# Kernel tuning notes

Measured on AMD Instinct MI355X. Metric: run time of the kernel, lower is better.

Reference implementation:

```python
import jax, jax.numpy as jnp
import numpy as np

HEAD_DIM = 64
N_HEADS = 12
N_KV_HEADS = 4
N_REP = N_HEADS // N_KV_HEADS  # 3


def _rope(x, cos, sin):
    # x: [B, S, H, D]; cos/sin: [1, S, D//2] -> broadcast over heads
    x2 = x.reshape(*x.shape[:-1], -1, 2)          # [B,S,H,D/2,2]
    x_r, x_i = x2[..., 0], x2[..., 1]
    c = cos[:, :, None, :]                         # [1,S,1,D/2]
    s = sin[:, :, None, :]
    o_r = x_r * c - x_i * s
    o_i = x_r * s + x_i * c
    return jnp.stack([o_r, o_i], axis=-1).reshape(x.shape)


def setup_inputs() -> dict:
    key = jax.random.key(0)
    ks = jax.random.split(key, 6)
    B, S, H = 4, 2048, 768
    hidden_state = jax.random.normal(ks[0], (B, S, H), dtype=jnp.float32)
    # true RoPE frequencies (theta=10000) for positions 0..S-1
    inv_freq = 1.0 / (10000.0 ** (np.arange(0, HEAD_DIM, 2, dtype=np.float32) / HEAD_DIM))
    ang = np.arange(S, dtype=np.float32)[:, None] * inv_freq[None, :]  # [S, D/2]
    freqs_cos = jnp.asarray(np.cos(ang))[None]     # [1,S,32]
    freqs_sin = jnp.asarray(np.sin(ang))[None]
    sc = 0.02
    wq = jax.random.normal(ks[1], (768, 768), dtype=jnp.float32) * sc
    wk = jax.random.normal(ks[2], (256, 768), dtype=jnp.float32) * sc
    wv = jax.random.normal(ks[3], (256, 768), dtype=jnp.float32) * sc
    wo = jax.random.normal(ks[4], (768, 768), dtype=jnp.float32) * sc
    return {"hidden_state": hidden_state, "freqs_cos": freqs_cos, "freqs_sin": freqs_sin,
            "wq": wq, "wk": wk, "wv": wv, "wo": wo}


def reference(hidden_state, freqs_cos, freqs_sin, wq, wk, wv, wo):
    B, S, _ = hidden_state.shape
    q = (hidden_state @ wq.T).reshape(B, S, N_HEADS, HEAD_DIM)
    k = (hidden_state @ wk.T).reshape(B, S, N_KV_HEADS, HEAD_DIM)
    v = (hidden_state @ wv.T).reshape(B, S, N_KV_HEADS, HEAD_DIM)
    q = _rope(q, freqs_cos, freqs_sin)
    k = _rope(k, freqs_cos, freqs_sin)
    # repeat_kv: [B,S,KV,D] -> [B,S,KV*n_rep,D]
    k = jnp.repeat(k, N_REP, axis=2)
    v = jnp.repeat(v, N_REP, axis=2)
    q = q.transpose(0, 2, 1, 3)  # [B,H,S,D]
    k = k.transpose(0, 2, 1, 3)
    v = v.transpose(0, 2, 1, 3)
    scores = jnp.einsum('bhqd,bhkd->bhqk', q, k) / np.sqrt(HEAD_DIM).astype(np.float32)
    mask = jnp.triu(jnp.full((S, S), -jnp.inf, dtype=scores.dtype), k=1)
    scores = scores + mask
    attn = jax.nn.softmax(scores.astype(jnp.float32), axis=-1).astype(q.dtype)
    # dropout is inference-off (identity)
    out = jnp.einsum('bhqk,bhkd->bhqd', attn, v)
    out = out.transpose(0, 2, 1, 3).reshape(B, S, N_HEADS * HEAD_DIM)
    return out @ wo.T, attn
```

## Files before the change

### kernel.cpp

```cpp
#include <hip/hip_runtime.h>
#include <hip/hip_bf16.h>
#include <stdint.h>


typedef __bf16 bf16x8 __attribute__((ext_vector_type(8)));
typedef float  f32x4  __attribute__((ext_vector_type(4)));

#define B_    4
#define S_    2048
#define H_    768
#define NH_Q  12
#define NKV_  4
#define D_    64
#define MROWS (B_ * S_)
#define NQKV  1280

__device__ __forceinline__ f32x4 mfma16(bf16x8 a, bf16x8 b, f32x4 c) {
  return __builtin_amdgcn_mfma_f32_16x16x32_bf16(a, b, c, 0, 0, 0);
}

__device__ __forceinline__ void st_nt4(float* p, f32x4 v) {
  __builtin_nontemporal_store(v, (f32x4*)p);
}

__device__ __forceinline__ uint32_t pk2(float a, float b) {
  __bf16 x = (__bf16)a, y = (__bf16)b;
  uint16_t xu = __builtin_bit_cast(uint16_t, x);
  uint16_t yu = __builtin_bit_cast(uint16_t, y);
  return (uint32_t)xu | ((uint32_t)yu << 16);
}
__device__ __forceinline__ float bl(uint32_t u) {
  uint32_t t = u << 16; return __builtin_bit_cast(float, t);
}
__device__ __forceinline__ float bh(uint32_t u) {
  uint32_t t = u & 0xffff0000u; return __builtin_bit_cast(float, t);
}

__global__ void cast_all(const float* __restrict__ X, const float* __restrict__ wq,
                         const float* __restrict__ wo, const float* __restrict__ wk,
                         const float* __restrict__ wv,
                         __bf16* __restrict__ Xb, __bf16* __restrict__ wqb,
                         __bf16* __restrict__ wob, __bf16* __restrict__ wkb,
                         __bf16* __restrict__ wvb) {
  int i = blockIdx.x * 256 + threadIdx.x;
  const int nX = MROWS * 768 / 8;
  const int nW = 768 * 768 / 8;
  const int nK = 256 * 768 / 8;
  const float* s; __bf16* d; int off;
  if (i < nX)                    { s = X;  d = Xb;  off = i; }
  else if (i < nX + nW)          { s = wq; d = wqb; off = i - nX; }
  else if (i < nX + 2 * nW)      { s = wo; d = wob; off = i - nX - nW; }
  else if (i < nX + 2 * nW + nK) { s = wk; d = wkb; off = i - nX - 2 * nW; }
  else if (i < nX + 2 * nW + 2 * nK) { s = wv; d = wvb; off = i - nX - 2 * nW - nK; }
  else return;
  const float4* sp = (const float4*)s + (size_t)off * 2;
  float4 a = sp[0], b = sp[1];
  bf16x8 o;
  o[0] = (__bf16)a.x; o[1] = (__bf16)a.y; o[2] = (__bf16)a.z; o[3] = (__bf16)a.w;
  o[4] = (__bf16)b.x; o[5] = (__bf16)b.y; o[6] = (__bf16)b.z; o[7] = (__bf16)b.w;
  *((bf16x8*)d + off) = o;
}

__global__ __launch_bounds__(256) void gemm_qkv(const __bf16* __restrict__ A,
                                                const __bf16* __restrict__ Wq,
                                                const __bf16* __restrict__ Wk,
                                                const __bf16* __restrict__ Wv,
                                                float* __restrict__ C) {
  const int K = 768;
  __shared__ __bf16 As[128 * 32];
  __shared__ __bf16 Bs[128 * 32];
  const int m0 = blockIdx.x * 128, n0 = blockIdx.y * 128;
  const __bf16* W;
  int nl;
  if (n0 < 768)       { W = Wq; nl = n0; }
  else if (n0 < 1024) { W = Wk; nl = n0 - 768; }
  else                { W = Wv; nl = n0 - 1024; }
  const int tid = threadIdx.x, lane = tid & 63, w = tid >> 6;
  const int wm = w >> 1, wn = w & 1;
  const int ql = lane & 15, grp = lane >> 4;
  const int srow = tid >> 1, shalf = tid & 1;
  const int sw = (srow >> 1) & 3;
  const int kc0 = (shalf * 2) ^ sw, kc1 = (shalf * 2 + 1) ^ sw;

  f32x4 acc[4][4] = {};

  for (int k0 = 0; k0 < K; k0 += 32) {
    bf16x8 av0 = *(const bf16x8*)(A + (size_t)(m0 + srow) * K + k0 + shalf * 16);
    bf16x8 av1 = *(const bf16x8*)(A + (size_t)(m0 + srow) * K + k0 + shalf * 16 + 8);
    bf16x8 bv0 = *(const bf16x8*)(W + (size_t)(nl + srow) * K + k0 + shalf * 16);
    bf16x8 bv1 = *(const bf16x8*)(W + (size_t)(nl + srow) * K + k0 + shalf * 16 + 8);
    __syncthreads();
    *(bf16x8*)(As + srow * 32 + kc0 * 8) = av0;
    *(bf16x8*)(As + srow * 32 + kc1 * 8) = av1;
    *(bf16x8*)(Bs + srow * 32 + kc0 * 8) = bv0;
    *(bf16x8*)(Bs + srow * 32 + kc1 * 8) = bv1;
    __syncthreads();

    bf16x8 af[4], bf_[4];
#pragma unroll
    for (int i = 0; i < 4; i++) {
      int row = wm * 64 + i * 16 + ql;
      int kc = grp ^ ((row >> 1) & 3);
      af[i] = *(const bf16x8*)(As + row * 32 + kc * 8);
    }
#pragma unroll
    for (int j = 0; j < 4; j++) {
      int row = wn * 64 + j * 16 + ql;
      int kc = grp ^ ((row >> 1) & 3);
      bf_[j] = *(const bf16x8*)(Bs + row * 32 + kc * 8);
    }
#pragma unroll
    for (int i = 0; i < 4; i++)
#pragma unroll
      for (int j = 0; j < 4; j++)
        acc[i][j] = mfma16(af[i], bf_[j], acc[i][j]);
  }

#pragma unroll
  for (int i = 0; i < 4; i++)
#pragma unroll
    for (int j = 0; j < 4; j++)
#pragma unroll
      for (int r = 0; r < 4; r++) {
        int row = m0 + wm * 64 + i * 16 + grp * 4 + r;
        int col = n0 + wn * 64 + j * 16 + ql;
        C[(size_t)row * NQKV + col] = acc[i][j][r];
      }
}

__global__ __launch_bounds__(256) void gemm_xwT(const __bf16* __restrict__ A,
                                                const __bf16* __restrict__ W,
                                                float* __restrict__ C,
                                                int M, int N, int K) {
  __shared__ __bf16 As[128 * 32];
  __shared__ __bf16 Bs[128 * 32];
  const int m0 = blockIdx.x * 128, n0 = blockIdx.y * 128;
  const int tid = threadIdx.x, lane = tid & 63, w = tid >> 6;
  const int wm = w >> 1, wn = w & 1;
  const int ql = lane & 15, grp = lane >> 4;
  const int srow = tid >> 1, shalf = tid & 1;
  const int sw = (srow >> 1) & 3;
  const int kc0 = (shalf * 2) ^ sw, kc1 = (shalf * 2 + 1) ^ sw;

  f32x4 acc[4][4] = {};

  for (int k0 = 0; k0 < K; k0 += 32) {
    bf16x8 av0 = *(const bf16x8*)(A + (size_t)(m0 + srow) * K + k0 + shalf * 16);
    bf16x8 av1 = *(const bf16x8*)(A + (size_t)(m0 + srow) * K + k0 + shalf * 16 + 8);
    bf16x8 bv0 = *(const bf16x8*)(W + (size_t)(n0 + srow) * K + k0 + shalf * 16);
    bf16x8 bv1 = *(const bf16x8*)(W + (size_t)(n0 + srow) * K + k0 + shalf * 16 + 8);
    __syncthreads();
    *(bf16x8*)(As + srow * 32 + kc0 * 8) = av0;
    *(bf16x8*)(As + srow * 32 + kc1 * 8) = av1;
    *(bf16x8*)(Bs + srow * 32 + kc0 * 8) = bv0;
    *(bf16x8*)(Bs + srow * 32 + kc1 * 8) = bv1;
    __syncthreads();

    bf16x8 af[4], bf_[4];
#pragma unroll
    for (int i = 0; i < 4; i++) {
      int row = wm * 64 + i * 16 + ql;
      int kc = grp ^ ((row >> 1) & 3);
      af[i] = *(const bf16x8*)(As + row * 32 + kc * 8);
    }
#pragma unroll
    for (int j = 0; j < 4; j++) {
      int row = wn * 64 + j * 16 + ql;
      int kc = grp ^ ((row >> 1) & 3);
      bf_[j] = *(const bf16x8*)(Bs + row * 32 + kc * 8);
    }
#pragma unroll
    for (int i = 0; i < 4; i++)
#pragma unroll
      for (int j = 0; j < 4; j++)
        acc[i][j] = mfma16(af[i], bf_[j], acc[i][j]);
  }

#pragma unroll
  for (int i = 0; i < 4; i++)
#pragma unroll
    for (int j = 0; j < 4; j++)
#pragma unroll
      for (int r = 0; r < 4; r++) {
        int row = m0 + wm * 64 + i * 16 + grp * 4 + r;
        int col = n0 + wn * 64 + j * 16 + ql;
        C[(size_t)row * N + col] = acc[i][j][r];
      }
}

__global__ void rope_both(const float* __restrict__ QKV, const float* __restrict__ fc,
                          const float* __restrict__ fs, __bf16* __restrict__ Qb,
                          __bf16* __restrict__ Kb) {
  int idx = blockIdx.x * 256 + threadIdx.x;
  const int NQp = MROWS * NH_Q * 32;
  int NH, colOff;
  __bf16* dst;
  float scale;
  if (idx < NQp) {
    NH = NH_Q; colOff = 0; dst = Qb; scale = 0.125f * 1.44269504f;
  } else {
    idx -= NQp;
    NH = NKV_; colOff = 768; dst = Kb; scale = 1.0f;
  }
  int t = idx & 31;
  int h = (idx >> 5) % NH;
  int row = idx / (32 * NH);
  int s = row & (S_ - 1), b = row >> 11;
  float x0 = QKV[(size_t)row * NQKV + colOff + h * 64 + 2 * t];
  float x1 = QKV[(size_t)row * NQKV + colOff + h * 64 + 2 * t + 1];
  float c = fc[s * 32 + t], sn = fs[s * 32 + t];
  float o0 = (x0 * c - x1 * sn) * scale;
  float o1 = (x0 * sn + x1 * c) * scale;
  __bf16* d = dst + (((size_t)(b * NH + h) * S_ + s) * 64 + 2 * t);
  d[0] = (__bf16)o0;
  d[1] = (__bf16)o1;
}

__global__ void transpose_v(const float* __restrict__ QKV, __bf16* __restrict__ VT) {
  __shared__ float tile[64][65];
  int rt = blockIdx.x;
  int ct = blockIdx.y;
  int r0 = rt * 64, c0 = ct * 64;
  int tx = threadIdx.x & 63, ty = threadIdx.x >> 6;
#pragma unroll
  for (int rep = 0; rep < 16; rep++) {
    int rr = rep * 4 + ty;
    tile[rr][tx] = QKV[(size_t)(r0 + rr) * NQKV + 1024 + c0 + tx];
  }
  __syncthreads();
  int b = r0 >> 11;
  int s0 = r0 & (S_ - 1);
#pragma unroll
  for (int rep = 0; rep < 16; rep++) {
    int dr = rep * 4 + ty;
    int d = c0 + dr;
    int kv = d >> 6, dd = d & 63;
    VT[(((size_t)(b * NKV_ + kv) * 64 + dd) * S_) + s0 + tx] = (__bf16)tile[tx][dr];
  }
}

template <int MAXC>
__device__ __forceinline__ void attn_part(
    int g, int b, int h, int w, int lane,
    const __bf16* __restrict__ Q, const __bf16* __restrict__ Kp,
    const __bf16* __restrict__ Vp, float* __restrict__ attn,
    __bf16* __restrict__ O, float (*lsum_s)[16], f32x4 (*obuf)[4]) {
  const int ql = lane & 15, grp = lane >> 4;
  const int qr0 = g * 16;
  const int nch = (g >> 1) + 1;
  const int i_q = qr0 + ql;
  const __bf16* Qp = Q + ((size_t)(b * NH_Q + h) * S_ + qr0) * 64;
  float* attnp = attn + ((size_t)(b * NH_Q + h) * S_ + qr0) * S_;

  bf16x8 bq0 = *(const bf16x8*)(Qp + ql * 64 + grp * 8);
  bf16x8 bq1 = *(const bf16x8*)(Qp + ql * 64 + 32 + grp * 8);

  uint32_t p[MAXC][4];
  float lsum = 0.f;
  f32x4 opv[4] = {};

#pragma unroll
  for (int c = 0; c < MAXC; c++) {
    const int j = w + 4 * c;
    if (j < nch) {
      const int j0 = j * 32;
      bf16x8 k0 = *(const bf16x8*)(Kp + (size_t)(j0 + ql) * 64 + grp * 8);
      bf16x8 k1 = *(const bf16x8*)(Kp + (size_t)(j0 + ql) * 64 + 32 + grp * 8);
      bf16x8 k2 = *(const bf16x8*)(Kp + (size_t)(j0 + 16 + ql) * 64 + grp * 8);
      bf16x8 k3 = *(const bf16x8*)(Kp + (size_t)(j0 + 16 + ql) * 64 + 32 + grp * 8);
      bf16x8 v0 = *(const bf16x8*)(Vp + (size_t)(0 * 16 + ql) * S_ + j0 + grp * 8);
      bf16x8 v1 = *(const bf16x8*)(Vp + (size_t)(1 * 16 + ql) * S_ + j0 + grp * 8);
      bf16x8 v2 = *(const bf16x8*)(Vp + (size_t)(2 * 16 + ql) * S_ + j0 + grp * 8);
      bf16x8 v3 = *(const bf16x8*)(Vp + (size_t)(3 * 16 + ql) * S_ + j0 + grp * 8);
      f32x4 s0 = {}, s1 = {};
      s0 = mfma16(k0, bq0, s0);
      s0 = mfma16(k1, bq1, s0);
      s1 = mfma16(k2, bq0, s1);
      s1 = mfma16(k3, bq1, s1);
      float e[8];
      if (j == nch - 1) {
#pragma unroll
        for (int r = 0; r < 4; r++) {
          int ja = j0 + grp * 4 + r, jb = j0 + 16 + grp * 4 + r;
          e[r]     = (ja <= i_q) ? exp2f(s0[r]) : 0.f;
          e[4 + r] = (jb <= i_q) ? exp2f(s1[r]) : 0.f;
        }
      } else {
#pragma unroll
        for (int r = 0; r < 4; r++) {
          e[r]     = exp2f(s0[r]);
          e[4 + r] = exp2f(s1[r]);
        }
      }
#pragma unroll
      for (int r = 0; r < 8; r++) lsum += e[r];
      p[c][0] = pk2(e[0], e[1]);
      p[c][1] = pk2(e[2], e[3]);
      p[c][2] = pk2(e[4], e[5]);
      p[c][3] = pk2(e[6], e[7]);

      int srcA = ql + 32 * (grp & 1);
      int srcB = srcA + 16;
      uint32_t A0 = __shfl(p[c][0], srcA), A1 = __shfl(p[c][1], srcA);
      uint32_t A2 = __shfl(p[c][2], srcA), A3 = __shfl(p[c][3], srcA);
      uint32_t B0 = __shfl(p[c][0], srcB), B1 = __shfl(p[c][1], srcB);
      uint32_t B2 = __shfl(p[c][2], srcB), B3 = __shfl(p[c][3], srcB);
      bool hi = (grp >> 1) != 0;
      union { bf16x8 v; uint32_t u[4]; } pu;
      pu.u[0] = hi ? A2 : A0;
      pu.u[1] = hi ? A3 : A1;
      pu.u[2] = hi ? B2 : B0;
      pu.u[3] = hi ? B3 : B1;
      opv[0] = mfma16(pu.v, v0, opv[0]);
      opv[1] = mfma16(pu.v, v1, opv[1]);
      opv[2] = mfma16(pu.v, v2, opv[2]);
      opv[3] = mfma16(pu.v, v3, opv[3]);
    }
  }

  lsum += __shfl_xor(lsum, 16);
  lsum += __shfl_xor(lsum, 32);
  if (lane < 16) lsum_s[w][ql] = lsum;
  f32x4* ob = obuf[w * 64 + lane];
  ob[0] = opv[0]; ob[1] = opv[1]; ob[2] = opv[2]; ob[3] = opv[3];
  __syncthreads();
  const float rinv = 1.f / (lsum_s[0][ql] + lsum_s[1][ql] + lsum_s[2][ql] + lsum_s[3][ql]);

  {
    const int dt = w;
    f32x4 acc = obuf[0 * 64 + lane][dt];
    acc += obuf[1 * 64 + lane][dt];
    acc += obuf[2 * 64 + lane][dt];
    acc += obuf[3 * 64 + lane][dt];
    __bf16* Op = O + ((size_t)(b * S_) + qr0) * H_ + h * 64;
#pragma unroll
    for (int r = 0; r < 4; r++) {
      int row = grp * 4 + r;
      float rr = 1.f / (lsum_s[0][row] + lsum_s[1][row] + lsum_s[2][row] + lsum_s[3][row]);
      Op[(size_t)row * H_ + dt * 16 + ql] = (__bf16)(acc[r] * rr);
    }
  }

#pragma unroll
  for (int c = 0; c < MAXC; c++) {
    const int j = w + 4 * c;
    if (j < nch) {
      const int j0 = j * 32;
      f32x4 q0, q1;
      q0[0] = bl(p[c][0]); q0[1] = bh(p[c][0]); q0[2] = bl(p[c][1]); q0[3] = bh(p[c][1]);
      q1[0] = bl(p[c][2]); q1[1] = bh(p[c][2]); q1[2] = bl(p[c][3]); q1[3] = bh(p[c][3]);
#pragma unroll
      for (int r = 0; r < 4; r++) { q0[r] *= rinv; q1[r] *= rinv; }
      st_nt4(attnp + (size_t)ql * S_ + j0 + grp * 4, q0);
      st_nt4(attnp + (size_t)ql * S_ + j0 + 16 + grp * 4, q1);
    }
  }

  const int jz = nch * 32;
  const int tid = w * 64 + lane;
  const f32x4 z4 = {0.f, 0.f, 0.f, 0.f};
#pragma unroll 1
  for (int rr = 0; rr < 16; rr++) {
    float* rowp = attnp + (size_t)rr * S_;
    for (int jj = jz + tid * 4; jj < S_; jj += 1024) st_nt4(rowp + jj, z4);
  }
  __syncthreads();
}

__global__ __launch_bounds__(256) void attn_kernel(const __bf16* __restrict__ Q,
                                                   const __bf16* __restrict__ Kb,
                                                   const __bf16* __restrict__ VT,
                                                   float* __restrict__ attn,
                                                   __bf16* __restrict__ O) {
  __shared__ float lsum_s[4][16];
  __shared__ f32x4 obuf[4 * 64][4];
  const int bid = blockIdx.x;
  const int r = bid & 7;
  const int qd = bid >> 3;
  const int x = qd & 63;
  const int idx6 = qd >> 6;
  const int g48 = idx6 * 8 + r;
  const int h = g48 >> 2, b = g48 & 3;
  const int lane = threadIdx.x & 63, w = threadIdx.x >> 6;
  const int kv = h / 3;
  const __bf16* Kp = Kb + (size_t)(b * NKV_ + kv) * S_ * 64;
  const __bf16* Vp = VT + (size_t)(b * NKV_ + kv) * 64 * S_;

  attn_part<8>(x, b, h, w, lane, Q, Kp, Vp, attn, O, lsum_s, obuf);
  attn_part<16>(127 - x, b, h, w, lane, Q, Kp, Vp, attn, O, lsum_s, obuf);
}

extern "C" void kernel_launch(void* const* d_in, const int* in_sizes, int n_in,
                              void* d_out, int out_size, void* d_ws, size_t ws_size,
                              hipStream_t stream) {
  (void)in_sizes; (void)n_in;
  const float* X  = (const float*)d_in[0];
  const float* fc = (const float*)d_in[1];
  const float* fs = (const float*)d_in[2];
  const float* wq = (const float*)d_in[3];
  const float* wk = (const float*)d_in[4];
  const float* wv = (const float*)d_in[5];
  const float* wo = (const float*)d_in[6];
  float* out0 = (float*)d_out;
  float* attn = out0 + (size_t)B_ * S_ * H_;

  char* p = (char*)d_ws;
  auto take = [&](size_t bytes) -> char* {
    char* r = p;
    p += (bytes + 255) & ~(size_t)255;
    return r;
  };
  __bf16* wqbf = (__bf16*)take((size_t)768 * 768 * 2);
  __bf16* wkbf = (__bf16*)take((size_t)256 * 768 * 2);
  __bf16* wvbf = (__bf16*)take((size_t)256 * 768 * 2);
  __bf16* wobf = (__bf16*)take((size_t)768 * 768 * 2);
  __bf16* Qbf  = (__bf16*)take((size_t)MROWS * 768 * 2);
  __bf16* Kbf  = (__bf16*)take((size_t)MROWS * 256 * 2);
  __bf16* VTbf = (__bf16*)take((size_t)MROWS * 256 * 2);
  __bf16* Obf  = (__bf16*)take((size_t)MROWS * 768 * 2);
  size_t used = (size_t)(p - (char*)d_ws);

  const size_t XBF_B  = (size_t)MROWS * 768 * 2;
  const size_t QKV_B  = (size_t)MROWS * NQKV * 4;
  const size_t TEMP_B = XBF_B + QKV_B;

  char* tp;
  if (used + TEMP_B + 1024 <= ws_size) {
    tp = p;
  } else {
    tp = (char*)(((uintptr_t)((char*)d_out + (size_t)out_size * 4 - TEMP_B)) & ~(uintptr_t)255);
  }
  __bf16* Xbf  = (__bf16*)tp;  tp += XBF_B;
  float*  QKVf = (float*)tp;

  {
    const int total8 = MROWS * 768 / 8 + 2 * (768 * 768 / 8) + 2 * (256 * 768 / 8);
    cast_all<<<(total8 + 255) / 256, 256, 0, stream>>>(X, wq, wo, wk, wv,
                                                       Xbf, wqbf, wobf, wkbf, wvbf);
  }

  gemm_qkv<<<dim3(MROWS / 128, NQKV / 128), 256, 0, stream>>>(Xbf, wqbf, wkbf, wvbf, QKVf);

  {
    const int totalPairs = MROWS * NH_Q * 32 + MROWS * NKV_ * 32;
    rope_both<<<(totalPairs + 255) / 256, 256, 0, stream>>>(QKVf, fc, fs, Qbf, Kbf);
  }
  transpose_v<<<dim3(MROWS / 64, 4), 256, 0, stream>>>(QKVf, VTbf);

  attn_kernel<<<dim3(48 * 64), 256, 0, stream>>>(Qbf, Kbf, VTbf, attn, Obf);

  gemm_xwT<<<dim3(MROWS / 128, 768 / 128), 256, 0, stream>>>(Obf, wobf, out0, MROWS, 768, 768);
}
```

Baseline: 323.0 us.

## Double-buffer GEMM tiles via direct global-to-LDS loads; split attention into two passes

The QKV and output projection GEMMs now use two LDS buffers filled by global_load_lds, so the next K tile loads while MFMAs run on the current one, and each K step needs one barrier instead of two. The attention row kernel now computes all exponentials and the row sum first, then in a second pass loads V, does the PV MFMAs and writes the normalized attention probabilities. The goal is to hide global latency in the GEMMs and interleave the large attention-matrix stores with compute. The cost is double the LDS per GEMM block, and a dependence on the direct-to-LDS lane layout matching the swizzle.

```diff
diff --git a/kernel.cpp b/kernel.cpp
--- a/kernel.cpp
+++ b/kernel.cpp
@@ -14,6 +14,7 @@
 #define D_    64
 #define MROWS (B_ * S_)
 #define NQKV  1280
+#define TILE_E (128 * 32)
 
 __device__ __forceinline__ f32x4 mfma16(bf16x8 a, bf16x8 b, f32x4 c) {
   return __builtin_amdgcn_mfma_f32_16x16x32_bf16(a, b, c, 0, 0, 0);
@@ -34,6 +35,12 @@
 }
 __device__ __forceinline__ float bh(uint32_t u) {
   uint32_t t = u & 0xffff0000u; return __builtin_bit_cast(float, t);
+}
+
+__device__ __forceinline__ void gload_lds16(const __bf16* g, __bf16* l) {
+  __builtin_amdgcn_global_load_lds(
+      (const __attribute__((address_space(1))) void*)g,
+      (__attribute__((address_space(3))) void*)l, 16, 0, 0);
 }
 
 __global__ void cast_all(const float* __restrict__ X, const float* __restrict__ wq,
@@ -61,131 +68,122 @@
   *((bf16x8*)d + off) = o;
 }
 
+struct GemmPtrs {
+  const __bf16 *gA0, *gA1, *gB0, *gB1;
+};
+
+__device__ __forceinline__ GemmPtrs make_ptrs(const __bf16* A, const __bf16* W,
+                                              int m0, int n0, int K, int tid) {
+  GemmPtrs gp;
+  int c0 = tid, c1 = 256 + tid;
+  int sr0 = c0 >> 2, kc0 = (c0 & 3) ^ ((sr0 >> 1) & 3);
+  int sr1 = c1 >> 2, kc1 = (c1 & 3) ^ ((sr1 >> 1) & 3);
+  gp.gA0 = A + (size_t)(m0 + sr0) * K + kc0 * 8;
+  gp.gA1 = A + (size_t)(m0 + sr1) * K + kc1 * 8;
+  gp.gB0 = W + (size_t)(n0 + sr0) * K + kc0 * 8;
+  gp.gB1 = W + (size_t)(n0 + sr1) * K + kc1 * 8;
+  return gp;
+}
+
+__device__ __forceinline__ void gemm_stage(GemmPtrs gp, int k0,
+                                           __bf16* As, __bf16* Bs, int tid) {
+  __bf16* lA0 = As + (size_t)(tid & ~63) * 8;
+  __bf16* lB0 = Bs + (size_t)(tid & ~63) * 8;
+  gload_lds16(gp.gA0 + k0, lA0);
+  gload_lds16(gp.gA1 + k0, lA0 + 256 * 8);
+  gload_lds16(gp.gB0 + k0, lB0);
+  gload_lds16(gp.gB1 + k0, lB0 + 256 * 8);
+}
+
+__device__ __forceinline__ void gemm_core(GemmPtrs gp, int K,
+                                          __bf16* As, __bf16* Bs,
+                                          int tid, f32x4 (*acc)[4]) {
+  const int lane = tid & 63, w = tid >> 6;
+  const int wm = w >> 1, wn = w & 1;
+  const int ql = lane & 15, grp = lane >> 4;
+
+  gemm_stage(gp, 0, As, Bs, tid);
+  __syncthreads();
+
+  const int nk = K / 32;
+  for (int ks = 0; ks < nk; ks++) {
+    __bf16* curA = As + (ks & 1) * TILE_E;
+    __bf16* curB = Bs + (ks & 1) * TILE_E;
+    if (ks + 1 < nk)
+      gemm_stage(gp, (ks + 1) * 32, As + ((ks + 1) & 1) * TILE_E,
+                 Bs + ((ks + 1) & 1) * TILE_E, tid);
+
+    bf16x8 af[4], bf_[4];
+#pragma unroll
+    for (int i = 0; i < 4; i++) {
+      int row = wm * 64 + i * 16 + ql;
+      int kc = grp ^ ((row >> 1) & 3);
+      af[i] = *(const bf16x8*)(curA + row * 32 + kc * 8);
+    }
+#pragma unroll
+    for (int j = 0; j < 4; j++) {
+      int row = wn * 64 + j * 16 + ql;
+      int kc = grp ^ ((row >> 1) & 3);
+      bf_[j] = *(const bf16x8*)(curB + row * 32 + kc * 8);
+    }
+#pragma unroll
+    for (int i = 0; i < 4; i++)
+#pragma unroll
+      for (int j = 0; j < 4; j++)
+        acc[i][j] = mfma16(af[i], bf_[j], acc[i][j]);
+    __syncthreads();
+  }
+}
+
+__device__ __forceinline__ void gemm_store(f32x4 (*acc)[4], float* C, int N,
+                                           int m0, int n0, int tid) {
+  const int lane = tid & 63, w = tid >> 6;
+  const int wm = w >> 1, wn = w & 1;
+  const int ql = lane & 15, grp = lane >> 4;
+#pragma unroll
+  for (int i = 0; i < 4; i++)
+#pragma unroll
+    for (int j = 0; j < 4; j++)
+#pragma unroll
+      for (int r = 0; r < 4; r++) {
+        int row = m0 + wm * 64 + i * 16 + grp * 4 + r;
+        int col = n0 + wn * 64 + j * 16 + ql;
+        C[(size_t)row * N + col] = acc[i][j][r];
+      }
+}
+
 __global__ __launch_bounds__(256) void gemm_qkv(const __bf16* __restrict__ A,
                                                 const __bf16* __restrict__ Wq,
                                                 const __bf16* __restrict__ Wk,
                                                 const __bf16* __restrict__ Wv,
                                                 float* __restrict__ C) {
-  const int K = 768;
-  __shared__ __bf16 As[128 * 32];
-  __shared__ __bf16 Bs[128 * 32];
+  __shared__ __bf16 As[2 * TILE_E];
+  __shared__ __bf16 Bs[2 * TILE_E];
   const int m0 = blockIdx.x * 128, n0 = blockIdx.y * 128;
   const __bf16* W;
   int nl;
   if (n0 < 768)       { W = Wq; nl = n0; }
   else if (n0 < 1024) { W = Wk; nl = n0 - 768; }
   else                { W = Wv; nl = n0 - 1024; }
-  const int tid = threadIdx.x, lane = tid & 63, w = tid >> 6;
-  const int wm = w >> 1, wn = w & 1;
-  const int ql = lane & 15, grp = lane >> 4;
-  const int srow = tid >> 1, shalf = tid & 1;
-  const int sw = (srow >> 1) & 3;
-  const int kc0 = (shalf * 2) ^ sw, kc1 = (shalf * 2 + 1) ^ sw;
-
+  const int tid = threadIdx.x;
   f32x4 acc[4][4] = {};
-
-  for (int k0 = 0; k0 < K; k0 += 32) {
-    bf16x8 av0 = *(const bf16x8*)(A + (size_t)(m0 + srow) * K + k0 + shalf * 16);
-    bf16x8 av1 = *(const bf16x8*)(A + (size_t)(m0 + srow) * K + k0 + shalf * 16 + 8);
-    bf16x8 bv0 = *(const bf16x8*)(W + (size_t)(nl + srow) * K + k0 + shalf * 16);
-    bf16x8 bv1 = *(const bf16x8*)(W + (size_t)(nl + srow) * K + k0 + shalf * 16 + 8);
-    __syncthreads();
-    *(bf16x8*)(As + srow * 32 + kc0 * 8) = av0;
-    *(bf16x8*)(As + srow * 32 + kc1 * 8) = av1;
-    *(bf16x8*)(Bs + srow * 32 + kc0 * 8) = bv0;
-    *(bf16x8*)(Bs + srow * 32 + kc1 * 8) = bv1;
-    __syncthreads();
-
-    bf16x8 af[4], bf_[4];
-#pragma unroll
-    for (int i = 0; i < 4; i++) {
-      int row = wm * 64 + i * 16 + ql;
-      int kc = grp ^ ((row >> 1) & 3);
-      af[i] = *(const bf16x8*)(As + row * 32 + kc * 8);
-    }
-#pragma unroll
-    for (int j = 0; j < 4; j++) {
-      int row = wn * 64 + j * 16 + ql;
-      int kc = grp ^ ((row >> 1) & 3);
-      bf_[j] = *(const bf16x8*)(Bs + row * 32 + kc * 8);
-    }
-#pragma unroll
-    for (int i = 0; i < 4; i++)
-#pragma unroll
-      for (int j = 0; j < 4; j++)
-        acc[i][j] = mfma16(af[i], bf_[j], acc[i][j]);
-  }
-
-#pragma unroll
-  for (int i = 0; i < 4; i++)
-#pragma unroll
-    for (int j = 0; j < 4; j++)
-#pragma unroll
-      for (int r = 0; r < 4; r++) {
-        int row = m0 + wm * 64 + i * 16 + grp * 4 + r;
-        int col = n0 + wn * 64 + j * 16 + ql;
-        C[(size_t)row * NQKV + col] = acc[i][j][r];
-      }
+  GemmPtrs gp = make_ptrs(A, W, m0, nl, 768, tid);
+  gemm_core(gp, 768, As, Bs, tid, acc);
+  gemm_store(acc, C, NQKV, m0, n0, tid);
 }
 
 __global__ __launch_bounds__(256) void gemm_xwT(const __bf16* __restrict__ A,
                                                 const __bf16* __restrict__ W,
                                                 float* __restrict__ C,
                                                 int M, int N, int K) {
-  __shared__ __bf16 As[128 * 32];
-  __shared__ __bf16 Bs[128 * 32];
+  __shared__ __bf16 As[2 * TILE_E];
+  __shared__ __bf16 Bs[2 * TILE_E];
   const int m0 = blockIdx.x * 128, n0 = blockIdx.y * 128;
-  const int tid = threadIdx.x, lane = tid & 63, w = tid >> 6;
-  const int wm = w >> 1, wn = w & 1;
-  const int ql = lane & 15, grp = lane >> 4;
-  const int srow = tid >> 1, shalf = tid & 1;
-  const int sw = (srow >> 1) & 3;
-  const int kc0 = (shalf * 2) ^ sw, kc1 = (shalf * 2 + 1) ^ sw;
-
+  const int tid = threadIdx.x;
   f32x4 acc[4][4] = {};
-
-  for (int k0 = 0; k0 < K; k0 += 32) {
-    bf16x8 av0 = *(const bf16x8*)(A + (size_t)(m0 + srow) * K + k0 + shalf * 16);
-    bf16x8 av1 = *(const bf16x8*)(A + (size_t)(m0 + srow) * K + k0 + shalf * 16 + 8);
-    bf16x8 bv0 = *(const bf16x8*)(W + (size_t)(n0 + srow) * K + k0 + shalf * 16);
-    bf16x8 bv1 = *(const bf16x8*)(W + (size_t)(n0 + srow) * K + k0 + shalf * 16 + 8);
-    __syncthreads();
-    *(bf16x8*)(As + srow * 32 + kc0 * 8) = av0;
-    *(bf16x8*)(As + srow * 32 + kc1 * 8) = av1;
-    *(bf16x8*)(Bs + srow * 32 + kc0 * 8) = bv0;
-    *(bf16x8*)(Bs + srow * 32 + kc1 * 8) = bv1;
-    __syncthreads();
-
-    bf16x8 af[4], bf_[4];
-#pragma unroll
-    for (int i = 0; i < 4; i++) {
-      int row = wm * 64 + i * 16 + ql;
-      int kc = grp ^ ((row >> 1) & 3);
-      af[i] = *(const bf16x8*)(As + row * 32 + kc * 8);
-    }
-#pragma unroll
-    for (int j = 0; j < 4; j++) {
-      int row = wn * 64 + j * 16 + ql;
-      int kc = grp ^ ((row >> 1) & 3);
-      bf_[j] = *(const bf16x8*)(Bs + row * 32 + kc * 8);
-    }
-#pragma unroll
-    for (int i = 0; i < 4; i++)
-#pragma unroll
-      for (int j = 0; j < 4; j++)
-        acc[i][j] = mfma16(af[i], bf_[j], acc[i][j]);
-  }
-
-#pragma unroll
-  for (int i = 0; i < 4; i++)
-#pragma unroll
-    for (int j = 0; j < 4; j++)
-#pragma unroll
-      for (int r = 0; r < 4; r++) {
-        int row = m0 + wm * 64 + i * 16 + grp * 4 + r;
-        int col = n0 + wn * 64 + j * 16 + ql;
-        C[(size_t)row * N + col] = acc[i][j][r];
-      }
+  GemmPtrs gp = make_ptrs(A, W, m0, n0, K, tid);
+  gemm_core(gp, K, As, Bs, tid, acc);
+  gemm_store(acc, C, N, m0, n0, tid);
 }
 
 __global__ void rope_both(const float* __restrict__ QKV, const float* __restrict__ fc,
@@ -257,7 +255,6 @@
 
   uint32_t p[MAXC][4];
   float lsum = 0.f;
-  f32x4 opv[4] = {};
 
 #pragma unroll
   for (int c = 0; c < MAXC; c++) {
@@ -268,10 +265,6 @@
       bf16x8 k1 = *(const bf16x8*)(Kp + (size_t)(j0 + ql) * 64 + 32 + grp * 8);
       bf16x8 k2 = *(const bf16x8*)(Kp + (size_t)(j0 + 16 + ql) * 64 + grp * 8);
       bf16x8 k3 = *(const bf16x8*)(Kp + (size_t)(j0 + 16 + ql) * 64 + 32 + grp * 8);
-      bf16x8 v0 = *(const bf16x8*)(Vp + (size_t)(0 * 16 + ql) * S_ + j0 + grp * 8);
-      bf16x8 v1 = *(const bf16x8*)(Vp + (size_t)(1 * 16 + ql) * S_ + j0 + grp * 8);
-      bf16x8 v2 = *(const bf16x8*)(Vp + (size_t)(2 * 16 + ql) * S_ + j0 + grp * 8);
-      bf16x8 v3 = *(const bf16x8*)(Vp + (size_t)(3 * 16 + ql) * S_ + j0 + grp * 8);
       f32x4 s0 = {}, s1 = {};
       s0 = mfma16(k0, bq0, s0);
       s0 = mfma16(k1, bq1, s0);
@@ -298,6 +291,33 @@
       p[c][1] = pk2(e[2], e[3]);
       p[c][2] = pk2(e[4], e[5]);
       p[c][3] = pk2(e[6], e[7]);
+    }
+  }
+
+  lsum += __shfl_xor(lsum, 16);
+  lsum += __shfl_xor(lsum, 32);
+  if (lane < 16) lsum_s[w][ql] = lsum;
+  __syncthreads();
+  const float rinv = 1.f / (lsum_s[0][ql] + lsum_s[1][ql] + lsum_s[2][ql] + lsum_s[3][ql]);
+
+  f32x4 opv[4] = {};
+#pragma unroll
+  for (int c = 0; c < MAXC; c++) {
+    const int j = w + 4 * c;
+    if (j < nch) {
+      const int j0 = j * 32;
+      bf16x8 v0 = *(const bf16x8*)(Vp + (size_t)(0 * 16 + ql) * S_ + j0 + grp * 8);
+      bf16x8 v1 = *(const bf16x8*)(Vp + (size_t)(1 * 16 + ql) * S_ + j0 + grp * 8);
+      bf16x8 v2 = *(const bf16x8*)(Vp + (size_t)(2 * 16 + ql) * S_ + j0 + grp * 8);
+      bf16x8 v3 = *(const bf16x8*)(Vp + (size_t)(3 * 16 + ql) * S_ + j0 + grp * 8);
+
+      f32x4 q0, q1;
+      q0[0] = bl(p[c][0]); q0[1] = bh(p[c][0]); q0[2] = bl(p[c][1]); q0[3] = bh(p[c][1]);
+      q1[0] = bl(p[c][2]); q1[1] = bh(p[c][2]); q1[2] = bl(p[c][3]); q1[3] = bh(p[c][3]);
+#pragma unroll
+      for (int r = 0; r < 4; r++) { q0[r] *= rinv; q1[r] *= rinv; }
+      st_nt4(attnp + (size_t)ql * S_ + j0 + grp * 4, q0);
+      st_nt4(attnp + (size_t)ql * S_ + j0 + 16 + grp * 4, q1);
 
       int srcA = ql + 32 * (grp & 1);
       int srcB = srcA + 16;
@@ -318,14 +338,9 @@
     }
   }
 
-  lsum += __shfl_xor(lsum, 16);
-  lsum += __shfl_xor(lsum, 32);
-  if (lane < 16) lsum_s[w][ql] = lsum;
   f32x4* ob = obuf[w * 64 + lane];
   ob[0] = opv[0]; ob[1] = opv[1]; ob[2] = opv[2]; ob[3] = opv[3];
   __syncthreads();
-  const float rinv = 1.f / (lsum_s[0][ql] + lsum_s[1][ql] + lsum_s[2][ql] + lsum_s[3][ql]);
-
   {
     const int dt = w;
     f32x4 acc = obuf[0 * 64 + lane][dt];
@@ -338,21 +353,6 @@
       int row = grp * 4 + r;
       float rr = 1.f / (lsum_s[0][row] + lsum_s[1][row] + lsum_s[2][row] + lsum_s[3][row]);
       Op[(size_t)row * H_ + dt * 16 + ql] = (__bf16)(acc[r] * rr);
-    }
-  }
-
-#pragma unroll
-  for (int c = 0; c < MAXC; c++) {
-    const int j = w + 4 * c;
-    if (j < nch) {
-      const int j0 = j * 32;
-      f32x4 q0, q1;
-      q0[0] = bl(p[c][0]); q0[1] = bh(p[c][0]); q0[2] = bl(p[c][1]); q0[3] = bh(p[c][1]);
-      q1[0] = bl(p[c][2]); q1[1] = bh(p[c][2]); q1[2] = bl(p[c][3]); q1[3] = bh(p[c][3]);
-#pragma unroll
-      for (int r = 0; r < 4; r++) { q0[r] *= rinv; q1[r] *= rinv; }
-      st_nt4(attnp + (size_t)ql * S_ + j0 + grp * 4, q0);
-      st_nt4(attnp + (size_t)ql * S_ + j0 + 16 + grp * 4, q1);
     }
   }
 
```

After: 292.7 us. -9.4%, faster.
